# Kernel optimization log

Hardware: AMD Instinct MI355X
Metric: run time of the kernel (lower is better)

The kernel has to match this reference:

```python
import jax, jax.numpy as jnp
from jax import lax
import numpy as np

N, T, HID, COMB, ATT, K, D = 128, 64, 512, 1024, 128, 20, 2
FMAP = 64  # CNN output channels; feature map is 14x14 -> 196 locations
ODIM = K + 2 * K * D + K + 1  # 121 mixture-density output params


def setup_inputs() -> dict:
    key = jax.random.key(0)
    keys = iter(jax.random.split(key, 64))

    def rn(shape, s=0.05):
        return jax.random.normal(next(keys), shape, jnp.float32) * s

    inp = dict(
        x=rn((N, T, D), 1.0),
        x_canv=jax.random.uniform(next(keys), (N, 1, 28, 28), dtype=jnp.float32),
        start=rn((N, D), 1.0),
        conv1_w=rn((16, 1, 3, 3), 0.3), conv1_b=rn((16,)),
        conv2_w=rn((32, 16, 3, 3), 0.1), conv2_b=rn((32,)),
        conv3_w=rn((64, 32, 3, 3), 0.1), conv3_b=rn((64,)),
        init_w=rn((2 * HID, FMAP + 16)), init_b=rn((2 * HID,)),
        Uw=rn((ATT, HID)), Ub=rn((ATT,)),
        Ww=rn((ATT, FMAP)), Wb=rn((ATT,)),
        vw=rn((1, ATT)), vb=rn((1,)),
        beta_w=rn((FMAP, HID)), beta_b=rn((FMAP,)),
        xemb_w=rn((16, D), 0.5), xemb_b=rn((16,)),
        semb_w=rn((16, D), 0.5), semb_b=rn((16,)),
        Wih=rn((4 * HID, FMAP + 16)), Whh=rn((4 * HID, HID)),
        bih=rn((4 * HID,)), bhh=rn((4 * HID,)),
        comb_w=rn((COMB, FMAP + HID + 32)), comb_b=rn((COMB,)),
        out_w=rn((ODIM, COMB)), out_b=rn((ODIM,)),
    )
    return inp


def _conv(x, w, b, stride):
    # torch Conv2d(kernel=3, padding=1) with NCHW / OIHW layout
    y = lax.conv_general_dilated(x, w, (stride, stride), ((1, 1), (1, 1)),
                                 dimension_numbers=('NCHW', 'OIHW', 'NCHW'))
    return y + b[None, :, None, None]


def reference(x, x_canv, start, conv1_w, conv1_b, conv2_w, conv2_b, conv3_w, conv3_b,
              init_w, init_b, Uw, Ub, Ww, Wb, vw, vb, beta_w, beta_b,
              xemb_w, xemb_b, semb_w, semb_b, Wih, Whh, bih, bhh,
              comb_w, comb_b, out_w, out_b):
    n, Tt, d = x.shape
    # sequence_pad: prepend zero vector, drop last step
    xp = jnp.concatenate([jnp.zeros((n, 1, d), x.dtype), x[:, :-1]], axis=1)
    xe = jnp.tanh(xp @ xemb_w.T + xemb_b)          # (n,T,16)
    se = jnp.tanh(start @ semb_w.T + semb_b)       # (n,16)
    # CNN (zscore_canvases with new_stats=True)
    c = (x_canv - 0.0243) / 0.1383
    c = jax.nn.relu(_conv(c, conv1_w, conv1_b, 1))
    c = jax.nn.relu(_conv(c, conv2_w, conv2_b, 1))
    c = jnp.tanh(_conv(c, conv3_w, conv3_b, 2))    # (n,64,14,14)
    a = c.transpose(0, 2, 3, 1).reshape(n, -1, FMAP)  # (n,196,64)
    # Initialize LSTM state (num_layers=1)
    hidden = jnp.tanh(jnp.concatenate([a.mean(axis=1), se], axis=1) @ init_w.T + init_b)
    hidden = hidden.reshape(n, HID, 2)
    h0, c0 = hidden[:, :, 0], hidden[:, :, 1]
    # AttendSAT.register_annotation: precompute W(a)
    W_a = a @ Ww.T + Wb                             # (n,196,att)
    # dropout masks are keep-probs (eval / dropout=0) -> all ones, identity

    def step(carry, xt):
        h, cs = carry
        Uh = h @ Uw.T + Ub                          # (n,att)
        e = (jnp.tanh(W_a + Uh[:, None, :]) @ vw.T).squeeze(-1) + vb[0]
        alpha = jax.nn.softmax(e, axis=-1)          # (n,196)
        z = jnp.einsum('nlf,nl->nf', a, alpha)      # (n,64)
        z = jax.nn.sigmoid(h @ beta_w.T + beta_b) * z
        gates = jnp.concatenate([xt, z], axis=1) @ Wih.T + bih + h @ Whh.T + bhh
        gi, gf, gg, go = jnp.split(gates, 4, axis=1)  # torch gate order i,f,g,o
        cs = jax.nn.sigmoid(gf) * cs + jax.nn.sigmoid(gi) * jnp.tanh(gg)
        h = jax.nn.sigmoid(go) * jnp.tanh(cs)
        y = jnp.tanh(jnp.concatenate([h, z, xt, se], axis=1) @ comb_w.T + comb_b)
        y = y @ out_w.T + out_b
        return (h, cs), y

    _, ys = lax.scan(step, (h0, c0), xe.transpose(1, 0, 2))
    y_out = ys.transpose(1, 0, 2)                   # (n,T,121)
    # unpack_output
    mix, means, scales, corrs, vlog = jnp.split(
        y_out, [K, K + K * D, K + 2 * K * D, 2 * K + 2 * K * D], axis=-1)
    mix = jax.nn.softmax(mix, axis=-1)
    means = means.reshape(n, Tt, K, D)
    scales = jnp.exp(scales).reshape(n, Tt, K, D)
    corrs = jnp.tanh(corrs)
    return (mix, means, scales, corrs, vlog.squeeze(-1))
```

## Files before the change

kernel.cpp:

```cpp
#include <hip/hip_runtime.h>


#define TN 128
#define TT 64

typedef __attribute__((ext_vector_type(4))) float f32x4;
typedef __attribute__((ext_vector_type(8))) short bf16x8;

__device__ __forceinline__ float fsigm(float x){ return __builtin_amdgcn_rcpf(1.0f + __expf(-x)); }
__device__ __forceinline__ float ftanh(float x){ return 1.0f - 2.0f*__builtin_amdgcn_rcpf(1.0f + __expf(2.0f*x)); }
__device__ __forceinline__ unsigned short f2bf(float f){
  unsigned int u = __float_as_uint(f);
  u += 0x7fffu + ((u >> 16) & 1u);
  return (unsigned short)(u >> 16);
}
__device__ __forceinline__ float b2f(unsigned short u){ return __uint_as_float(((unsigned)u)<<16); }

__global__ __launch_bounds__(256) void k_conv1(const float* __restrict__ xc, const float* __restrict__ w,
                                               const float* __restrict__ b, float* __restrict__ c1){
  int idx = blockIdx.x*256 + threadIdx.x;
  if (idx >= TN*16*784) return;
  int p = idx % 784, oc = (idx/784) & 15, n = idx/(784*16);
  int py = p/28, px = p%28;
  const float* src = xc + n*784;
  float acc = b[oc];
  #pragma unroll
  for (int ky=0;ky<3;ky++){
    int iy = py+ky-1; if (iy<0||iy>=28) continue;
    #pragma unroll
    for (int kx=0;kx<3;kx++){
      int ix = px+kx-1; if (ix<0||ix>=28) continue;
      acc += (src[iy*28+ix]-0.0243f)*(1.0f/0.1383f) * w[oc*9+ky*3+kx];
    }
  }
  c1[idx] = fmaxf(acc, 0.0f);
}

__global__ __launch_bounds__(256) void k_im2col2(const float* __restrict__ c1, unsigned short* __restrict__ a2){
  int idx = blockIdx.x*256 + threadIdx.x;
  int k = idx % 160, r = idx / 160;
  unsigned short v = 0;
  if (k < 144){
    int ic = k/9, rem = k - ic*9, ky = rem/3, kx = rem - ky*3;
    int p = r % 784, n = r / 784;
    int py = p/28, px = p%28;
    int iy = py+ky-1, ix = px+kx-1;
    if (iy>=0 && iy<28 && ix>=0 && ix<28) v = f2bf(c1[(n*16+ic)*784 + iy*28+ix]);
  }
  a2[idx] = v;
}

__global__ __launch_bounds__(256) void k_gconv2(const unsigned short* __restrict__ a2,
    const unsigned short* __restrict__ w2b, const float* __restrict__ b2,
    unsigned short* __restrict__ c2bf){
  int mbase = blockIdx.x*128;
  int tid = threadIdx.x, w = tid>>6, l = tid&63;
  int lr = l&15, lk = (l>>4)*8;
  __shared__ unsigned short at[128*168];
  {
    int row = tid>>1, off = (tid&1)*80;
    const unsigned short* sp = a2 + (size_t)(mbase+row)*160 + off;
    #pragma unroll
    for (int j=0;j<10;j++) *(float4*)&at[row*168 + off + j*8] = *(const float4*)(sp + j*8);
  }
  __syncthreads();
  f32x4 acc[2][2];
  #pragma unroll
  for (int mi=0;mi<2;mi++){ acc[mi][0]=(f32x4){0,0,0,0}; acc[mi][1]=(f32x4){0,0,0,0}; }
  for (int kt=0; kt<5; ++kt){
    bf16x8 b0 = *(const bf16x8*)(w2b + (0*16+lr)*160 + kt*32 + lk);
    bf16x8 b1 = *(const bf16x8*)(w2b + (1*16+lr)*160 + kt*32 + lk);
    #pragma unroll
    for (int mi=0;mi<2;mi++){
      bf16x8 afrag = *(const bf16x8*)&at[((2*w+mi)*16+lr)*168 + kt*32 + lk];
      acc[mi][0] = __builtin_amdgcn_mfma_f32_16x16x32_bf16(afrag, b0, acc[mi][0], 0,0,0);
      acc[mi][1] = __builtin_amdgcn_mfma_f32_16x16x32_bf16(afrag, b1, acc[mi][1], 0,0,0);
    }
  }
  #pragma unroll
  for (int mi=0;mi<2;mi++){
    #pragma unroll
    for (int j=0;j<2;j++){
      int oc = j*16 + lr;
      float bb = b2[oc];
      #pragma unroll
      for (int i=0;i<4;i++){
        int r = mbase + (2*w+mi)*16 + (l>>4)*4 + i;
        c2bf[(size_t)r*32 + oc] = f2bf(fmaxf(acc[mi][j][i] + bb, 0.0f));
      }
    }
  }
}

__global__ __launch_bounds__(256) void k_im2col3(const unsigned short* __restrict__ c2bf, unsigned short* __restrict__ a3){
  int idx = blockIdx.x*256 + threadIdx.x;
  int k = idx % 320, r = idx / 320;
  unsigned short v = 0;
  if (k < 288){
    int ic = k/9, rem = k - ic*9, ky = rem/3, kx = rem - ky*3;
    int p = r % 196, n = r / 196;
    int py = p/14, px = p%14;
    int iy = 2*py+ky-1, ix = 2*px+kx-1;
    if (iy>=0 && iy<28 && ix>=0 && ix<28) v = c2bf[(size_t)(n*784 + iy*28+ix)*32 + ic];
  }
  a3[idx] = v;
}

__global__ __launch_bounds__(256) void k_gconv3(const unsigned short* __restrict__ a3,
    const unsigned short* __restrict__ w3b, const float* __restrict__ b3,
    unsigned short* __restrict__ afbf, unsigned short* __restrict__ abf){
  int mbase = blockIdx.x*128;
  int tid = threadIdx.x, w = tid>>6, l = tid&63;
  int lr = l&15, lk = (l>>4)*8;
  __shared__ unsigned short at[128*168];
  f32x4 acc[2][4];
  #pragma unroll
  for (int mi=0;mi<2;mi++)
    #pragma unroll
    for (int j=0;j<4;j++) acc[mi][j]=(f32x4){0,0,0,0};
  for (int kt2=0; kt2<2; ++kt2){
    {
      int row = tid>>1, off = (tid&1)*80;
      const unsigned short* sp = a3 + (size_t)(mbase+row)*320 + kt2*160 + off;
      #pragma unroll
      for (int j=0;j<10;j++) *(float4*)&at[row*168 + off + j*8] = *(const float4*)(sp + j*8);
    }
    __syncthreads();
    for (int kt=0; kt<5; ++kt){
      #pragma unroll
      for (int mi=0;mi<2;mi++){
        bf16x8 afrag = *(const bf16x8*)&at[((2*w+mi)*16+lr)*168 + kt*32 + lk];
        #pragma unroll
        for (int j=0;j<4;j++){
          bf16x8 bf = *(const bf16x8*)(w3b + (size_t)(j*16+lr)*320 + kt2*160 + kt*32 + lk);
          acc[mi][j] = __builtin_amdgcn_mfma_f32_16x16x32_bf16(afrag, bf, acc[mi][j], 0,0,0);
        }
      }
    }
    __syncthreads();
  }
  #pragma unroll
  for (int mi=0;mi<2;mi++){
    #pragma unroll
    for (int j=0;j<4;j++){
      int oc = j*16 + lr;
      float bb = b3[oc];
      #pragma unroll
      for (int i=0;i<4;i++){
        int r = mbase + (2*w+mi)*16 + (l>>4)*4 + i;
        int n = r/196, p = r - n*196;
        float v = ftanh(acc[mi][j][i] + bb);
        unsigned short vb16 = f2bf(v);
        afbf[(size_t)(n*64+oc)*196 + p] = vb16;
        abf[(size_t)r*64 + oc] = vb16;
      }
    }
  }
}

__global__ __launch_bounds__(64) void k_amean(const unsigned short* __restrict__ afbf, float* __restrict__ amean){
  int n = blockIdx.x, f = threadIdx.x;
  const unsigned short* row = afbf + (size_t)(n*64+f)*196;
  float s = 0;
  for (int l=0;l<196;l++) s += b2f(row[l]);
  amean[n*64+f] = s * (1.0f/196.0f);
}

__global__ __launch_bounds__(256) void k_embed(const float* __restrict__ x, const float* __restrict__ start,
    const float* __restrict__ xw, const float* __restrict__ xb,
    const float* __restrict__ sw, const float* __restrict__ sb,
    float* __restrict__ xe, float* __restrict__ se){
  int idx = blockIdx.x*256 + threadIdx.x;
  if (idx < TN*TT*16){
    int j = idx & 15, t = (idx>>4) & 63, n = idx>>10;
    float acc = xb[j];
    if (t > 0){
      const float* xp = x + (n*TT + t-1)*2;
      acc += xp[0]*xw[j*2] + xp[1]*xw[j*2+1];
    }
    xe[idx] = ftanh(acc);
  } else if (idx < TN*TT*16 + TN*16){
    int k2 = idx - TN*TT*16;
    int j = k2 & 15, n = k2 >> 4;
    float acc = sb[j] + start[n*2]*sw[j*2] + start[n*2+1]*sw[j*2+1];
    se[k2] = ftanh(acc);
  }
}

__global__ __launch_bounds__(256) void k_init(const float* __restrict__ amean, const float* __restrict__ se,
    const float* __restrict__ w, const float* __restrict__ b,
    unsigned short* __restrict__ hbfA, float* __restrict__ cbuf){
  int idx = blockIdx.x*256 + threadIdx.x;
  if (idx >= TN*1024) return;
  int o = idx & 1023, n = idx >> 10;
  const float* wr = w + o*80;
  float acc = b[o];
  for (int k2=0;k2<64;k2++) acc += amean[n*64+k2]*wr[k2];
  for (int k2=0;k2<16;k2++) acc += se[n*16+k2]*wr[64+k2];
  float v = ftanh(acc);
  if (o & 1) cbuf[n*512 + (o>>1)] = v;
  else       hbfA[n*512 + (o>>1)] = f2bf(v);
}

__global__ __launch_bounds__(256) void k_prep(
    const float* __restrict__ Whh, const float* __restrict__ Wih,
    const float* __restrict__ bih, const float* __restrict__ bhh,
    const float* __restrict__ comb_w, const float* __restrict__ out_w, const float* __restrict__ out_b,
    const float* __restrict__ Uw, const float* __restrict__ beta_w, const float* __restrict__ Ww,
    const float* __restrict__ conv2_w, const float* __restrict__ conv3_w,
    unsigned short* __restrict__ wgf, float* __restrict__ gbias,
    unsigned short* __restrict__ cwbf, unsigned short* __restrict__ owbf, float* __restrict__ obias,
    unsigned short* __restrict__ uwbf, unsigned short* __restrict__ betabf, unsigned short* __restrict__ wwbf,
    unsigned short* __restrict__ w2b, unsigned short* __restrict__ w3b){
  int idx = blockIdx.x*256 + threadIdx.x;
  if (idx < 1245184){
    int fragi = idx >> 9;
    int lane8 = idx & 511;
    int lane = lane8 >> 3, j = lane8 & 7;
    int g = fragi / 608;
    int rem = fragi - g*608;
    int b = rem / 19, kt = rem - b*19;
    int row = g*512 + b*16 + (lane & 15);
    int col = kt*32 + (lane >> 4)*8 + j;
    float v = 0.f;
    if (col < 512) v = Whh[(size_t)row*512 + col];
    else { int c2 = col - 512; if (c2 < 80) v = Wih[(size_t)row*80 + c2]; }
    wgf[idx] = f2bf(v);
    return;
  }
  idx -= 1245184;
  if (idx < 2048){ gbias[idx] = bih[idx]+bhh[idx]; return; }
  idx -= 2048;
  if (idx < 622592){ cwbf[idx] = f2bf(comb_w[idx]); return; }
  idx -= 622592;
  if (idx < 131072){ int o = idx>>10, k2 = idx & 1023; owbf[idx] = (o<121)? f2bf(out_w[o*1024+k2]) : (unsigned short)0; return; }
  idx -= 131072;
  if (idx < 128){ obias[idx] = (idx<121)? out_b[idx] : 0.0f; return; }
  idx -= 128;
  if (idx < 65536){ uwbf[idx] = f2bf(Uw[idx]); return; }
  idx -= 65536;
  if (idx < 32768){ betabf[idx] = f2bf(beta_w[idx]); return; }
  idx -= 32768;
  if (idx < 8192){ wwbf[idx] = f2bf(Ww[idx]); return; }
  idx -= 8192;
  if (idx < 5120){ int o = idx/160, k2 = idx - o*160; w2b[idx] = (k2<144)? f2bf(conv2_w[o*144+k2]) : (unsigned short)0; return; }
  idx -= 5120;
  if (idx < 20480){ int o = idx/320, k2 = idx - o*320; w3b[idx] = (k2<288)? f2bf(conv3_w[o*320-o*320+o*320]) : (unsigned short)0;  }
  if (idx < 20480){ int o = idx/320, k2 = idx - o*320; w3b[idx] = (k2<288)? f2bf(conv3_w[o*288+k2]) : (unsigned short)0; return; }
}

__global__ __launch_bounds__(256) void k_wa(const unsigned short* __restrict__ abf,
    const unsigned short* __restrict__ wwbf, const float* __restrict__ Wb,
    unsigned short* __restrict__ wabf){
  int mbase = blockIdx.x*128;
  int tid = threadIdx.x, w = tid>>6, l = tid&63;
  int lr = l & 15, lk = (l>>4)*8;
  __shared__ unsigned short at[128*40];
  f32x4 acc[8][2];
  #pragma unroll
  for (int m=0;m<8;m++){ acc[m][0] = (f32x4){0,0,0,0}; acc[m][1] = (f32x4){0,0,0,0}; }
  for (int kt=0; kt<2; ++kt){
    int row = tid>>1, half = (tid&1)*16;
    const unsigned short* sp = abf + (mbase+row)*64 + kt*32 + half;
    *(float4*)&at[row*40 + half]     = *(const float4*)sp;
    *(float4*)&at[row*40 + half + 8] = *(const float4*)(sp + 8);
    __syncthreads();
    bf16x8 b0 = *(const bf16x8*)(wwbf + ((2*w+0)*16 + lr)*64 + kt*32 + lk);
    bf16x8 b1 = *(const bf16x8*)(wwbf + ((2*w+1)*16 + lr)*64 + kt*32 + lk);
    #pragma unroll
    for (int m=0;m<8;m++){
      bf16x8 afrag = *(const bf16x8*)&at[(m*16+lr)*40 + lk];
      acc[m][0] = __builtin_amdgcn_mfma_f32_16x16x32_bf16(afrag, b0, acc[m][0], 0,0,0);
      acc[m][1] = __builtin_amdgcn_mfma_f32_16x16x32_bf16(afrag, b1, acc[m][1], 0,0,0);
    }
    __syncthreads();
  }
  #pragma unroll
  for (int m=0;m<8;m++){
    #pragma unroll
    for (int j=0;j<2;j++){
      int att = (2*w+j)*16 + lr;
      float wb = Wb[att];
      #pragma unroll
      for (int i=0;i<4;i++){
        int arow = mbase + m*16 + (l>>4)*4 + i;
        int n = arow/196, l2 = arow - n*196;
        wabf[((size_t)n*196 + l2)*128 + att] = f2bf(acc[m][j][i] + wb);
      }
    }
  }
}

__global__ __launch_bounds__(512) void k_stepA(int t,
    const unsigned short* __restrict__ hbf_in,
    const unsigned short* __restrict__ uwbf, const float* __restrict__ Ub,
    const unsigned short* __restrict__ betabf, const float* __restrict__ beta_b,
    const float* __restrict__ vw, const float* __restrict__ vb,
    const unsigned short* __restrict__ wabf, const unsigned short* __restrict__ afbf,
    unsigned short* __restrict__ ubf_all, unsigned short* __restrict__ cbf,
    const unsigned short* __restrict__ wgf, float* __restrict__ gpart)
{
  const int bid = blockIdx.x, tid = threadIdx.x;
  __shared__ __align__(16) float hs[512];
  __shared__ __align__(16) float Uh[128];
  __shared__ __align__(16) float vws[128];
  __shared__ float bsig[64];
  __shared__ float ew[196];
  __shared__ float red[16];
  __shared__ float up[4][128];
  __shared__ float qp8[8][64];
  __shared__ float ep2[256][2];
  __shared__ __align__(16) unsigned short at2[2][128*36];

  if (bid < TN){
    const int n = bid;
    hs[tid] = b2f(hbf_in[n*512 + tid]);
    if (tid < 128) vws[tid] = vw[tid];
    const float vb0 = vb[0];
    __syncthreads();
    {
      int att = tid & 127, q = tid >> 7;
      const unsigned short* uw = uwbf + (size_t)att*512 + q*128;
      const float* hh = hs + q*128;
      float acc = 0.f;
      #pragma unroll 4
      for (int k=0;k<128;k+=8){
        bf16x8 v = *(const bf16x8*)(uw + k);
        acc += hh[k+0]*b2f(v[0]) + hh[k+1]*b2f(v[1]) + hh[k+2]*b2f(v[2]) + hh[k+3]*b2f(v[3])
             + hh[k+4]*b2f(v[4]) + hh[k+5]*b2f(v[5]) + hh[k+6]*b2f(v[6]) + hh[k+7]*b2f(v[7]);
      }
      up[q][att] = acc;
    }
    {
      int f = tid & 63, q = tid >> 6;
      const unsigned short* bw = betabf + (size_t)f*512 + q*64;
      const float* hh = hs + q*64;
      float acc = 0.f;
      #pragma unroll 4
      for (int k=0;k<64;k+=8){
        bf16x8 v = *(const bf16x8*)(bw + k);
        acc += hh[k+0]*b2f(v[0]) + hh[k+1]*b2f(v[1]) + hh[k+2]*b2f(v[2]) + hh[k+3]*b2f(v[3])
             + hh[k+4]*b2f(v[4]) + hh[k+5]*b2f(v[5]) + hh[k+6]*b2f(v[6]) + hh[k+7]*b2f(v[7]);
      }
      qp8[q][f] = acc;
    }
    __syncthreads();
    if (tid < 128) Uh[tid] = Ub[tid] + up[0][tid]+up[1][tid]+up[2][tid]+up[3][tid];
    else if (tid < 192){
      int f = tid-128;
      bsig[f] = fsigm(beta_b[f] + qp8[0][f]+qp8[1][f]+qp8[2][f]+qp8[3][f]
                                + qp8[4][f]+qp8[5][f]+qp8[6][f]+qp8[7][f]);
    }
    __syncthreads();
    {
      int l = tid >> 1, half = tid & 1;
      float acc = 0.f;
      if (l < 196){
        const unsigned short* wr = wabf + ((size_t)n*196 + l)*128 + half*64;
        const float* uh = Uh + half*64;
        const float* vv = vws + half*64;
        #pragma unroll 2
        for (int k=0;k<64;k+=8){
          bf16x8 wv = *(const bf16x8*)(wr + k);
          acc += vv[k+0]*ftanh(b2f(wv[0]) + uh[k+0]) + vv[k+1]*ftanh(b2f(wv[1]) + uh[k+1])
               + vv[k+2]*ftanh(b2f(wv[2]) + uh[k+2]) + vv[k+3]*ftanh(b2f(wv[3]) + uh[k+3])
               + vv[k+4]*ftanh(b2f(wv[4]) + uh[k+4]) + vv[k+5]*ftanh(b2f(wv[5]) + uh[k+5])
               + vv[k+6]*ftanh(b2f(wv[6]) + uh[k+6]) + vv[k+7]*ftanh(b2f(wv[7]) + uh[k+7]);
        }
      }
      ep2[l][half] = acc;
    }
    __syncthreads();
    float ev = -1e30f;
    if (tid < 196) ev = vb0 + ep2[tid][0] + ep2[tid][1];
    float m = ev;
    #pragma unroll
    for (int off=32; off>0; off>>=1) m = fmaxf(m, __shfl_xor(m, off));
    if ((tid&63)==0) red[tid>>6] = m;
    __syncthreads();
    float mx = red[0];
    #pragma unroll
    for (int i=1;i<8;i++) mx = fmaxf(mx, red[i]);
    float ex = (tid<196) ? __expf(ev - mx) : 0.0f;
    float ss = ex;
    #pragma unroll
    for (int off=32; off>0; off>>=1) ss += __shfl_xor(ss, off);
    if ((tid&63)==0) red[8+(tid>>6)] = ss;
    if (tid<196) ew[tid] = ex;
    __syncthreads();
    float inv = __builtin_amdgcn_rcpf(red[8]+red[9]+red[10]+red[11]+red[12]+red[13]+red[14]+red[15]);
    {
      int f = tid & 63, q = tid >> 6;
      int l0 = q*25, l1 = (l0+25 < 196) ? l0+25 : 196;
      const unsigned short* an = afbf + (size_t)n*12544 + (size_t)f*196;
      float acc = 0.f;
      for (int l2=l0; l2<l1; l2++) acc += ew[l2]*b2f(an[l2]);
      qp8[q][f] = acc;
    }
    __syncthreads();
    if (tid < 64){
      float z = bsig[tid]*(qp8[0][tid]+qp8[1][tid]+qp8[2][tid]+qp8[3][tid]
                          +qp8[4][tid]+qp8[5][tid]+qp8[6][tid]+qp8[7][tid])*inv;
      unsigned short zb = f2bf(z);
      ubf_all[((size_t)t*TN + n)*96 + 16 + tid] = zb;
      cbf[((size_t)n*TT + t)*608 + 512 + tid] = zb;
    }
  } else {
    const int b = bid - TN;
    const int w = tid>>6, l = tid&63, lr = l&15, li = l>>4, lk = li*8;
    const int g = w & 3, mh = w >> 2;
    bf16x8 wreg[16];
    {
      const unsigned short* wp = wgf + ((size_t)(g*32 + b)*19)*512 + (size_t)l*8;
      #pragma unroll
      for (int i=0;i<16;i++) wreg[i] = *(const bf16x8*)(wp + (size_t)i*512);
    }
    f32x4 acc[4];
    #pragma unroll
    for (int m2=0;m2<4;m2++) acc[m2] = (f32x4){0,0,0,0};
    {
      int row = tid>>2, seg = (tid&3)*8;
      *(float4*)&at2[0][row*36+seg] = *(const float4*)(hbf_in + (size_t)row*512 + seg);
    }
    __syncthreads();
    for (int kt=0; kt<16; ++kt){
      if (kt+1 < 16){
        int row = tid>>2, seg = (tid&3)*8;
        *(float4*)&at2[(kt+1)&1][row*36+seg] = *(const float4*)(hbf_in + (size_t)row*512 + (kt+1)*32 + seg);
      }
      #pragma unroll
      for (int m2=0;m2<4;m2++){
        bf16x8 a = *(const bf16x8*)&at2[kt&1][((mh*4+m2)*16 + lr)*36 + lk];
        acc[m2] = __builtin_amdgcn_mfma_f32_16x16x32_bf16(a, wreg[kt], acc[m2], 0,0,0);
      }
      __syncthreads();
    }
    #pragma unroll
    for (int m2=0;m2<4;m2++){
      #pragma unroll
      for (int i=0;i<4;i++){
        int n2 = (mh*4+m2)*16 + li*4 + i;
        gpart[(((size_t)g*128 + n2)<<9) + b*16 + lr] = acc[m2][i];
      }
    }
  }
}

__global__ __launch_bounds__(256) void k_stepB(int t,
    unsigned short* __restrict__ hout,
    const unsigned short* __restrict__ ubf_all,
    const unsigned short* __restrict__ wgf, const float* __restrict__ gbias,
    const float* __restrict__ gpart,
    float* __restrict__ cbuf, unsigned short* __restrict__ cbf)
{
  const int b = blockIdx.x, tid = threadIdx.x;
  const int w = tid>>6, l = tid&63, lr = l&15, li = l>>4, lk = li*8;
  __shared__ float gsh[4][128][16];
  __shared__ __align__(16) unsigned short at[128*100];
  const unsigned short* ub = ubf_all + (size_t)t*TN*96;
  for (int i = tid; i < 2048; i += 256){
    int g = i>>9, r = i&511, n2 = r>>2, j4 = r&3;
    *(float4*)&gsh[g][n2][j4*4] = *(const float4*)&gpart[(((size_t)g*128 + n2)<<9) + b*16 + j4*4];
  }
  for (int i = tid; i < 1536; i += 256){
    int row = i/12, c8 = i - row*12;
    *(float4*)&at[row*100 + c8*8] = *(const float4*)(ub + (size_t)row*96 + c8*8);
  }
  bf16x8 wz[3];
  {
    const unsigned short* wp = wgf + (((size_t)(w*32 + b)*19) + 16)*512 + (size_t)l*8;
    #pragma unroll
    for (int i=0;i<3;i++) wz[i] = *(const bf16x8*)(wp + (size_t)i*512);
  }
  f32x4 acc[8];
  #pragma unroll
  for (int m=0;m<8;m++) acc[m] = (f32x4){0,0,0,0};
  __syncthreads();
  #pragma unroll
  for (int kt=0; kt<3; ++kt){
    #pragma unroll
    for (int m=0;m<8;m++){
      bf16x8 a = *(const bf16x8*)&at[(m*16+lr)*100 + kt*32 + lk];
      acc[m] = __builtin_amdgcn_mfma_f32_16x16x32_bf16(a, wz[kt], acc[m], 0,0,0);
    }
  }
  #pragma unroll
  for (int m=0;m<8;m++)
    #pragma unroll
    for (int i=0;i<4;i++)
      gsh[w][m*16 + li*4 + i][lr] += acc[m][i];
  __syncthreads();
  #pragma unroll
  for (int e=0;e<8;++e){
    int c = tid*8 + e;
    int nn = c>>4, j = c&15;
    int hidx = b*16 + j;
    float gi = gsh[0][nn][j] + gbias[         hidx];
    float gf = gsh[1][nn][j] + gbias[1*512 + hidx];
    float gg = gsh[2][nn][j] + gbias[2*512 + hidx];
    float go = gsh[3][nn][j] + gbias[3*512 + hidx];
    float cc = cbuf[nn*512 + hidx];
    float cs = fsigm(gf)*cc + fsigm(gi)*ftanh(gg);
    float h  = fsigm(go)*ftanh(cs);
    cbuf[nn*512 + hidx] = cs;
    unsigned short hb = f2bf(h);
    hout[nn*512 + hidx] = hb;
    cbf[((size_t)nn*TT + t)*608 + hidx] = hb;
  }
}

__global__ __launch_bounds__(256) void k_cbf_xs(const float* __restrict__ xe, const float* __restrict__ se,
                                                unsigned short* __restrict__ cbf,
                                                unsigned short* __restrict__ ubf_all){
  int idx = blockIdx.x*256 + threadIdx.x;
  if (idx >= TN*TT*64) return;
  int j = idx & 63, r = idx >> 6;
  int n = r >> 6, t = r & 63;
  if (j < 16)      cbf[(size_t)r*608 + 576 + j] = f2bf(xe[r*16 + j]);
  else if (j < 32) cbf[(size_t)r*608 + 592 + (j-16)] = f2bf(se[n*16 + (j-16)]);
  else if (j < 48) ubf_all[((size_t)t*TN + n)*96 + (j-32)] = f2bf(xe[r*16 + (j-32)]);
  else             ubf_all[((size_t)t*TN + n)*96 + 80 + (j-48)] = 0;
}

__global__ __launch_bounds__(256) void k_comb(const unsigned short* __restrict__ cbf,
    const unsigned short* __restrict__ cwbf, const float* __restrict__ comb_b,
    unsigned short* __restrict__ ybf){
  int mbase = blockIdx.x*128, obase = blockIdx.y*128;
  int tid = threadIdx.x, w = tid>>6, l = tid&63;
  int lr = l&15, lk = (l>>4)*8;
  __shared__ unsigned short at[128*40];
  f32x4 acc[8][2];
  #pragma unroll
  for (int m=0;m<8;m++){ acc[m][0] = (f32x4){0,0,0,0}; acc[m][1] = (f32x4){0,0,0,0}; }
  for (int kt=0; kt<19; ++kt){
    int row = tid>>1, half = (tid&1)*16;
    const unsigned short* sp = cbf + (size_t)(mbase+row)*608 + kt*32 + half;
    *(float4*)&at[row*40 + half]     = *(const float4*)sp;
    *(float4*)&at[row*40 + half + 8] = *(const float4*)(sp + 8);
    __syncthreads();
    bf16x8 b0 = *(const bf16x8*)(cwbf + (size_t)(obase + (2*w+0)*16 + lr)*608 + kt*32 + lk);
    bf16x8 b1 = *(const bf16x8*)(cwbf + (size_t)(obase + (2*w+1)*16 + lr)*608 + kt*32 + lk);
    #pragma unroll
    for (int m=0;m<8;m++){
      bf16x8 afrag = *(const bf16x8*)&at[(m*16+lr)*40 + lk];
      acc[m][0] = __builtin_amdgcn_mfma_f32_16x16x32_bf16(afrag, b0, acc[m][0], 0,0,0);
      acc[m][1] = __builtin_amdgcn_mfma_f32_16x16x32_bf16(afrag, b1, acc[m][1], 0,0,0);
    }
    __syncthreads();
  }
  #pragma unroll
  for (int m=0;m<8;m++){
    #pragma unroll
    for (int j=0;j<2;j++){
      int o = obase + (2*w+j)*16 + lr;
      float cb = comb_b[o];
      #pragma unroll
      for (int i=0;i<4;i++){
        int r = mbase + m*16 + (l>>4)*4 + i;
        ybf[(size_t)r*1024 + o] = f2bf(ftanh(acc[m][j][i] + cb));
      }
    }
  }
}

__global__ __launch_bounds__(256) void k_out(const unsigned short* __restrict__ ybf,
    const unsigned short* __restrict__ owbf, const float* __restrict__ obias,
    float* __restrict__ obuf){
  int mbase = blockIdx.x*128;
  int tid = threadIdx.x, w = tid>>6, l = tid&63;
  int lr = l&15, lk = (l>>4)*8;
  __shared__ unsigned short at[128*40];
  f32x4 acc[8][2];
  #pragma unroll
  for (int m=0;m<8;m++){ acc[m][0] = (f32x4){0,0,0,0}; acc[m][1] = (f32x4){0,0,0,0}; }
  for (int kt=0; kt<32; ++kt){
    int row = tid>>1, half = (tid&1)*16;
    const unsigned short* sp = ybf + (size_t)(mbase+row)*1024 + kt*32 + half;
    *(float4*)&at[row*40 + half]     = *(const float4*)sp;
    *(float4*)&at[row*40 + half + 8] = *(const float4*)(sp + 8);
    __syncthreads();
    bf16x8 b0 = *(const bf16x8*)(owbf + ((2*w+0)*16 + lr)*1024 + kt*32 + lk);
    bf16x8 b1 = *(const bf16x8*)(owbf + ((2*w+1)*16 + lr)*1024 + kt*32 + lk);
    #pragma unroll
    for (int m=0;m<8;m++){
      bf16x8 afrag = *(const bf16x8*)&at[(m*16+lr)*40 + lk];
      acc[m][0] = __builtin_amdgcn_mfma_f32_16x16x32_bf16(afrag, b0, acc[m][0], 0,0,0);
      acc[m][1] = __builtin_amdgcn_mfma_f32_16x16x32_bf16(afrag, b1, acc[m][1], 0,0,0);
    }
    __syncthreads();
  }
  #pragma unroll
  for (int m=0;m<8;m++){
    #pragma unroll
    for (int j=0;j<2;j++){
      int o = (2*w+j)*16 + lr;
      float ob = obias[o];
      #pragma unroll
      for (int i=0;i<4;i++){
        int r = mbase + m*16 + (l>>4)*4 + i;
        obuf[(size_t)r*128 + o] = acc[m][j][i] + ob;
      }
    }
  }
}

__global__ __launch_bounds__(256) void k_post(const float* __restrict__ obuf, float* __restrict__ out){
  int r = blockIdx.x*256 + threadIdx.x;
  if (r >= TN*TT) return;
  const float* row = obuf + (size_t)r*128;
  float mx = -1e30f;
  #pragma unroll
  for (int k2=0;k2<20;k2++) mx = fmaxf(mx, row[k2]);
  float e[20]; float s = 0;
  #pragma unroll
  for (int k2=0;k2<20;k2++){ e[k2] = __expf(row[k2]-mx); s += e[k2]; }
  float inv = __builtin_amdgcn_rcpf(s);
  float* mixo  = out;
  float* meano = out + 163840;
  float* scaleo= out + 491520;
  float* corro = out + 819200;
  float* vlogo = out + 983040;
  #pragma unroll
  for (int k2=0;k2<20;k2++) mixo[r*20+k2] = e[k2]*inv;
  #pragma unroll
  for (int j=0;j<40;j++) meano[r*40+j] = row[20+j];
  #pragma unroll
  for (int j=0;j<40;j++) scaleo[r*40+j] = __expf(row[60+j]);
  #pragma unroll
  for (int k2=0;k2<20;k2++) corro[r*20+k2] = ftanh(row[100+k2]);
  vlogo[r] = row[120];
}

extern "C" void kernel_launch(void* const* d_in, const int* in_sizes, int n_in,
                              void* d_out, int out_size, void* d_ws, size_t ws_size,
                              hipStream_t stream){
  const float* x       = (const float*)d_in[0];
  const float* x_canv  = (const float*)d_in[1];
  const float* start_  = (const float*)d_in[2];
  const float* conv1_w = (const float*)d_in[3];
  const float* conv1_b = (const float*)d_in[4];
  const float* conv2_w = (const float*)d_in[5];
  const float* conv2_b = (const float*)d_in[6];
  const float* conv3_w = (const float*)d_in[7];
  const float* conv3_b = (const float*)d_in[8];
  const float* init_w  = (const float*)d_in[9];
  const float* init_b  = (const float*)d_in[10];
  const float* Uw      = (const float*)d_in[11];
  const float* Ub      = (const float*)d_in[12];
  const float* Ww      = (const float*)d_in[13];
  const float* Wb      = (const float*)d_in[14];
  const float* vw      = (const float*)d_in[15];
  const float* vb      = (const float*)d_in[16];
  const float* beta_w  = (const float*)d_in[17];
  const float* beta_b  = (const float*)d_in[18];
  const float* xemb_w  = (const float*)d_in[19];
  const float* xemb_b  = (const float*)d_in[20];
  const float* semb_w  = (const float*)d_in[21];
  const float* semb_b  = (const float*)d_in[22];
  const float* Wih     = (const float*)d_in[23];
  const float* Whh     = (const float*)d_in[24];
  const float* bih     = (const float*)d_in[25];
  const float* bhh     = (const float*)d_in[26];
  const float* comb_w  = (const float*)d_in[27];
  const float* comb_b  = (const float*)d_in[28];
  const float* out_w   = (const float*)d_in[29];
  const float* out_b   = (const float*)d_in[30];
  (void)in_sizes; (void)n_in; (void)out_size; (void)ws_size;

  char* wsb = (char*)d_ws;
  size_t off = 0;
  auto alloc = [&](size_t bytes)->char*{
    char* p = wsb + off;
    off = (off + bytes + 255) & ~(size_t)255;
    return p;
  };
  float*          c1     = (float*)alloc((size_t)TN*16*784*4);
  unsigned short* a2     = (unsigned short*)alloc((size_t)100352*160*2);
  unsigned short* a3     = a2;
  unsigned short* c2bf   = (unsigned short*)alloc((size_t)100352*32*2);
  unsigned short* afbf   = (unsigned short*)alloc((size_t)TN*64*196*2);
  unsigned short* abf    = (unsigned short*)alloc((size_t)TN*196*64*2);
  float*          amean  = (float*)alloc((size_t)TN*64*4);
  float*          xe     = (float*)alloc((size_t)TN*TT*16*4);
  float*          se     = (float*)alloc((size_t)TN*16*4);
  unsigned short* wabf   = (unsigned short*)alloc((size_t)TN*196*128*2);
  float*          cbuf   = (float*)alloc((size_t)TN*512*4);
  unsigned short* hbfA   = (unsigned short*)alloc((size_t)TN*512*2);
  unsigned short* hbfB   = (unsigned short*)alloc((size_t)TN*512*2);
  unsigned short* ubf_all= (unsigned short*)alloc((size_t)TT*TN*96*2);
  unsigned short* cbf    = (unsigned short*)alloc((size_t)TN*TT*608*2);
  unsigned short* ybf    = (unsigned short*)alloc((size_t)TN*TT*1024*2);
  float*          obuf   = (float*)alloc((size_t)TN*TT*128*4);
  unsigned short* wgf    = (unsigned short*)alloc((size_t)1245184*2);
  float*          gbias  = (float*)alloc((size_t)2048*4);
  float*          gpart  = (float*)alloc((size_t)4*128*512*4);
  unsigned short* cwbf   = (unsigned short*)alloc((size_t)1024*608*2);
  unsigned short* owbf   = (unsigned short*)alloc((size_t)128*1024*2);
  float*          obias  = (float*)alloc((size_t)128*4);
  unsigned short* uwbf   = (unsigned short*)alloc((size_t)128*512*2);
  unsigned short* betabf = (unsigned short*)alloc((size_t)64*512*2);
  unsigned short* wwbf   = (unsigned short*)alloc((size_t)128*64*2);
  unsigned short* w2b    = (unsigned short*)alloc((size_t)32*160*2);
  unsigned short* w3b    = (unsigned short*)alloc((size_t)64*320*2);

  hipLaunchKernelGGL(k_conv1, dim3(6272), dim3(256), 0, stream, x_canv, conv1_w, conv1_b, c1);
  hipLaunchKernelGGL(k_prep, dim3(8334), dim3(256), 0, stream,
                     Whh, Wih, bih, bhh, comb_w, out_w, out_b, Uw, beta_w, Ww, conv2_w, conv3_w,
                     wgf, gbias, cwbf, owbf, obias, uwbf, betabf, wwbf, w2b, w3b);
  hipLaunchKernelGGL(k_im2col2, dim3(62720), dim3(256), 0, stream, c1, a2);
  hipLaunchKernelGGL(k_gconv2, dim3(784), dim3(256), 0, stream, a2, w2b, conv2_b, c2bf);
  hipLaunchKernelGGL(k_im2col3, dim3(31360), dim3(256), 0, stream, c2bf, a3);
  hipLaunchKernelGGL(k_gconv3, dim3(196), dim3(256), 0, stream, a3, w3b, conv3_b, afbf, abf);
  hipLaunchKernelGGL(k_amean, dim3(128), dim3(64), 0, stream, afbf, amean);
  hipLaunchKernelGGL(k_embed, dim3(520), dim3(256), 0, stream, x, start_, xemb_w, xemb_b, semb_w, semb_b, xe, se);
  hipLaunchKernelGGL(k_init, dim3(512), dim3(256), 0, stream, amean, se, init_w, init_b, hbfA, cbuf);
  hipLaunchKernelGGL(k_wa, dim3(196), dim3(256), 0, stream, abf, wwbf, Wb, wabf);
  hipLaunchKernelGGL(k_cbf_xs, dim3(2048), dim3(256), 0, stream, xe, se, cbf, ubf_all);

  for (int t = 0; t < TT; ++t){
    unsigned short* hin  = (t & 1) ? hbfB : hbfA;
    unsigned short* hout = (t & 1) ? hbfA : hbfB;
    hipLaunchKernelGGL(k_stepA, dim3(160), dim3(512), 0, stream, t,
                       hin, uwbf, Ub, betabf, beta_b, vw, vb, wabf, afbf, ubf_all, cbf, wgf, gpart);
    hipLaunchKernelGGL(k_stepB, dim3(32), dim3(256), 0, stream, t,
                       hout, ubf_all, wgf, gbias, gpart, cbuf, cbf);
  }

  hipLaunchKernelGGL(k_comb, dim3(64, 8), dim3(256), 0, stream, cbf, cwbf, comb_b, ybf);
  hipLaunchKernelGGL(k_out, dim3(64), dim3(256), 0, stream, ybf, owbf, obias, obuf);
  hipLaunchKernelGGL(k_post, dim3(32), dim3(256), 0, stream, obuf, (float*)d_out);
}
```

Before: 1.670 ms.

## Fuse im2col into conv GEMM kernels and read hidden state directly in stepA

Removes the separate im2col kernels for conv2 and conv3. The GEMM kernels now gather their input patches straight from the bf16 activations into shared memory, which avoids writing and re-reading large im2col buffers in global memory. conv1 now writes bf16 output, halving its store size. In stepA, the fp32 shared-memory copy of h and its barrier are dropped, and the bf16 h vectors are read directly from global memory. In exchange, the gather becomes scalar, with per-element index math and uncoalesced reads inside the GEMM kernels.

```diff
diff --git a/kernel.cpp b/kernel.cpp
--- a/kernel.cpp
+++ b/kernel.cpp
@@ -17,7 +17,7 @@
 __device__ __forceinline__ float b2f(unsigned short u){ return __uint_as_float(((unsigned)u)<<16); }
 
 __global__ __launch_bounds__(256) void k_conv1(const float* __restrict__ xc, const float* __restrict__ w,
-                                               const float* __restrict__ b, float* __restrict__ c1){
+                                               const float* __restrict__ b, unsigned short* __restrict__ c1bf){
   int idx = blockIdx.x*256 + threadIdx.x;
   if (idx >= TN*16*784) return;
   int p = idx % 784, oc = (idx/784) & 15, n = idx/(784*16);
@@ -33,24 +33,10 @@
       acc += (src[iy*28+ix]-0.0243f)*(1.0f/0.1383f) * w[oc*9+ky*3+kx];
     }
   }
-  c1[idx] = fmaxf(acc, 0.0f);
-}
-
-__global__ __launch_bounds__(256) void k_im2col2(const float* __restrict__ c1, unsigned short* __restrict__ a2){
-  int idx = blockIdx.x*256 + threadIdx.x;
-  int k = idx % 160, r = idx / 160;
-  unsigned short v = 0;
-  if (k < 144){
-    int ic = k/9, rem = k - ic*9, ky = rem/3, kx = rem - ky*3;
-    int p = r % 784, n = r / 784;
-    int py = p/28, px = p%28;
-    int iy = py+ky-1, ix = px+kx-1;
-    if (iy>=0 && iy<28 && ix>=0 && ix<28) v = f2bf(c1[(n*16+ic)*784 + iy*28+ix]);
-  }
-  a2[idx] = v;
-}
-
-__global__ __launch_bounds__(256) void k_gconv2(const unsigned short* __restrict__ a2,
+  c1bf[idx] = f2bf(fmaxf(acc, 0.0f));
+}
+
+__global__ __launch_bounds__(256) void k_gconv2(const unsigned short* __restrict__ c1bf,
     const unsigned short* __restrict__ w2b, const float* __restrict__ b2,
     unsigned short* __restrict__ c2bf){
   int mbase = blockIdx.x*128;
@@ -59,9 +45,19 @@
   __shared__ unsigned short at[128*168];
   {
     int row = tid>>1, off = (tid&1)*80;
-    const unsigned short* sp = a2 + (size_t)(mbase+row)*160 + off;
-    #pragma unroll
-    for (int j=0;j<10;j++) *(float4*)&at[row*168 + off + j*8] = *(const float4*)(sp + j*8);
+    int r = mbase + row;
+    int p = r % 784, n = r / 784;
+    int py = p/28, px = p%28;
+    for (int kk=0; kk<80; ++kk){
+      int k = off + kk;
+      unsigned short v = 0;
+      if (k < 144){
+        int ic = k/9, rem = k - ic*9, ky = rem/3, kx = rem - ky*3;
+        int iy = py+ky-1, ix = px+kx-1;
+        if (iy>=0 && iy<28 && ix>=0 && ix<28) v = c1bf[(n*16+ic)*784 + iy*28+ix];
+      }
+      at[row*168 + k] = v;
+    }
   }
   __syncthreads();
   f32x4 acc[2][2];
@@ -92,21 +88,7 @@
   }
 }
 
-__global__ __launch_bounds__(256) void k_im2col3(const unsigned short* __restrict__ c2bf, unsigned short* __restrict__ a3){
-  int idx = blockIdx.x*256 + threadIdx.x;
-  int k = idx % 320, r = idx / 320;
-  unsigned short v = 0;
-  if (k < 288){
-    int ic = k/9, rem = k - ic*9, ky = rem/3, kx = rem - ky*3;
-    int p = r % 196, n = r / 196;
-    int py = p/14, px = p%14;
-    int iy = 2*py+ky-1, ix = 2*px+kx-1;
-    if (iy>=0 && iy<28 && ix>=0 && ix<28) v = c2bf[(size_t)(n*784 + iy*28+ix)*32 + ic];
-  }
-  a3[idx] = v;
-}
-
-__global__ __launch_bounds__(256) void k_gconv3(const unsigned short* __restrict__ a3,
+__global__ __launch_bounds__(256) void k_gconv3(const unsigned short* __restrict__ c2bf,
     const unsigned short* __restrict__ w3b, const float* __restrict__ b3,
     unsigned short* __restrict__ afbf, unsigned short* __restrict__ abf){
   int mbase = blockIdx.x*128;
@@ -118,12 +100,20 @@
   for (int mi=0;mi<2;mi++)
     #pragma unroll
     for (int j=0;j<4;j++) acc[mi][j]=(f32x4){0,0,0,0};
+  int srow = tid>>1, soff = (tid&1)*80;
+  int sr = mbase + srow;
+  int sp2 = sr % 196, sn = sr / 196;
+  int spy = sp2/14, spx = sp2%14;
   for (int kt2=0; kt2<2; ++kt2){
-    {
-      int row = tid>>1, off = (tid&1)*80;
-      const unsigned short* sp = a3 + (size_t)(mbase+row)*320 + kt2*160 + off;
-      #pragma unroll
-      for (int j=0;j<10;j++) *(float4*)&at[row*168 + off + j*8] = *(const float4*)(sp + j*8);
+    for (int kk=0; kk<80; ++kk){
+      int k = kt2*160 + soff + kk;
+      unsigned short v = 0;
+      if (k < 288){
+        int ic = k/9, rem = k - ic*9, ky = rem/3, kx = rem - ky*3;
+        int iy = 2*spy+ky-1, ix = 2*spx+kx-1;
+        if (iy>=0 && iy<28 && ix>=0 && ix<28) v = c2bf[(size_t)(sn*784 + iy*28+ix)*32 + ic];
+      }
+      at[srow*168 + soff + kk] = v;
     }
     __syncthreads();
     for (int kt=0; kt<5; ++kt){
@@ -245,7 +235,6 @@
   idx -= 8192;
   if (idx < 5120){ int o = idx/160, k2 = idx - o*160; w2b[idx] = (k2<144)? f2bf(conv2_w[o*144+k2]) : (unsigned short)0; return; }
   idx -= 5120;
-  if (idx < 20480){ int o = idx/320, k2 = idx - o*320; w3b[idx] = (k2<288)? f2bf(conv3_w[o*320-o*320+o*320]) : (unsigned short)0;  }
   if (idx < 20480){ int o = idx/320, k2 = idx - o*320; w3b[idx] = (k2<288)? f2bf(conv3_w[o*288+k2]) : (unsigned short)0; return; }
 }
 
@@ -301,7 +290,6 @@
     const unsigned short* __restrict__ wgf, float* __restrict__ gpart)
 {
   const int bid = blockIdx.x, tid = threadIdx.x;
-  __shared__ __align__(16) float hs[512];
   __shared__ __align__(16) float Uh[128];
   __shared__ __align__(16) float vws[128];
   __shared__ float bsig[64];
@@ -314,33 +302,33 @@
 
   if (bid < TN){
     const int n = bid;
-    hs[tid] = b2f(hbf_in[n*512 + tid]);
     if (tid < 128) vws[tid] = vw[tid];
     const float vb0 = vb[0];
-    __syncthreads();
     {
       int att = tid & 127, q = tid >> 7;
       const unsigned short* uw = uwbf + (size_t)att*512 + q*128;
-      const float* hh = hs + q*128;
+      const unsigned short* hh = hbf_in + (size_t)n*512 + q*128;
       float acc = 0.f;
       #pragma unroll 4
       for (int k=0;k<128;k+=8){
         bf16x8 v = *(const bf16x8*)(uw + k);
-        acc += hh[k+0]*b2f(v[0]) + hh[k+1]*b2f(v[1]) + hh[k+2]*b2f(v[2]) + hh[k+3]*b2f(v[3])
-             + hh[k+4]*b2f(v[4]) + hh[k+5]*b2f(v[5]) + hh[k+6]*b2f(v[6]) + hh[k+7]*b2f(v[7]);
+        bf16x8 hv = *(const bf16x8*)(hh + k);
+        acc += b2f(hv[0])*b2f(v[0]) + b2f(hv[1])*b2f(v[1]) + b2f(hv[2])*b2f(v[2]) + b2f(hv[3])*b2f(v[3])
+             + b2f(hv[4])*b2f(v[4]) + b2f(hv[5])*b2f(v[5]) + b2f(hv[6])*b2f(v[6]) + b2f(hv[7])*b2f(v[7]);
       }
       up[q][att] = acc;
     }
     {
       int f = tid & 63, q = tid >> 6;
       const unsigned short* bw = betabf + (size_t)f*512 + q*64;
-      const float* hh = hs + q*64;
+      const unsigned short* hh = hbf_in + (size_t)n*512 + q*64;
       float acc = 0.f;
       #pragma unroll 4
       for (int k=0;k<64;k+=8){
         bf16x8 v = *(const bf16x8*)(bw + k);
-        acc += hh[k+0]*b2f(v[0]) + hh[k+1]*b2f(v[1]) + hh[k+2]*b2f(v[2]) + hh[k+3]*b2f(v[3])
-             + hh[k+4]*b2f(v[4]) + hh[k+5]*b2f(v[5]) + hh[k+6]*b2f(v[6]) + hh[k+7]*b2f(v[7]);
+        bf16x8 hv = *(const bf16x8*)(hh + k);
+        acc += b2f(hv[0])*b2f(v[0]) + b2f(hv[1])*b2f(v[1]) + b2f(hv[2])*b2f(v[2]) + b2f(hv[3])*b2f(v[3])
+             + b2f(hv[4])*b2f(v[4]) + b2f(hv[5])*b2f(v[5]) + b2f(hv[6])*b2f(v[6]) + b2f(hv[7])*b2f(v[7]);
       }
       qp8[q][f] = acc;
     }
@@ -674,9 +662,7 @@
     off = (off + bytes + 255) & ~(size_t)255;
     return p;
   };
-  float*          c1     = (float*)alloc((size_t)TN*16*784*4);
-  unsigned short* a2     = (unsigned short*)alloc((size_t)100352*160*2);
-  unsigned short* a3     = a2;
+  unsigned short* c1bf   = (unsigned short*)alloc((size_t)TN*16*784*2);
   unsigned short* c2bf   = (unsigned short*)alloc((size_t)100352*32*2);
   unsigned short* afbf   = (unsigned short*)alloc((size_t)TN*64*196*2);
   unsigned short* abf    = (unsigned short*)alloc((size_t)TN*196*64*2);
@@ -703,14 +689,12 @@
   unsigned short* w2b    = (unsigned short*)alloc((size_t)32*160*2);
   unsigned short* w3b    = (unsigned short*)alloc((size_t)64*320*2);
 
-  hipLaunchKernelGGL(k_conv1, dim3(6272), dim3(256), 0, stream, x_canv, conv1_w, conv1_b, c1);
+  hipLaunchKernelGGL(k_conv1, dim3(6272), dim3(256), 0, stream, x_canv, conv1_w, conv1_b, c1bf);
   hipLaunchKernelGGL(k_prep, dim3(8334), dim3(256), 0, stream,
                      Whh, Wih, bih, bhh, comb_w, out_w, out_b, Uw, beta_w, Ww, conv2_w, conv3_w,
                      wgf, gbias, cwbf, owbf, obias, uwbf, betabf, wwbf, w2b, w3b);
-  hipLaunchKernelGGL(k_im2col2, dim3(62720), dim3(256), 0, stream, c1, a2);
-  hipLaunchKernelGGL(k_gconv2, dim3(784), dim3(256), 0, stream, a2, w2b, conv2_b, c2bf);
-  hipLaunchKernelGGL(k_im2col3, dim3(31360), dim3(256), 0, stream, c2bf, a3);
-  hipLaunchKernelGGL(k_gconv3, dim3(196), dim3(256), 0, stream, a3, w3b, conv3_b, afbf, abf);
+  hipLaunchKernelGGL(k_gconv2, dim3(784), dim3(256), 0, stream, c1bf, w2b, conv2_b, c2bf);
+  hipLaunchKernelGGL(k_gconv3, dim3(196), dim3(256), 0, stream, c2bf, w3b, conv3_b, afbf, abf);
   hipLaunchKernelGGL(k_amean, dim3(128), dim3(64), 0, stream, afbf, amean);
   hipLaunchKernelGGL(k_embed, dim3(520), dim3(256), 0, stream, x, start_, xemb_w, xemb_b, semb_w, semb_b, xe, se);
   hipLaunchKernelGGL(k_init, dim3(512), dim3(256), 0, stream, amean, se, init_w, init_b, hbfA, cbuf);
```

New measurement: 1.750 ms. +4.8%, slower.
